# Kernel optimization log

Hardware: AMD Instinct MI355X
Metric: run time of the kernel (lower is better)

## Reference

```python
import jax, jax.numpy as jnp
import numpy as np

B, C, H, W = 32, 64, 64, 64
K, D = 512, 64
COMMITMENT_COST = 0.25


def setup_inputs() -> dict:
    key = jax.random.key(0)
    k1, k2, k3 = jax.random.split(key, 3)
    inputs = jax.random.normal(k1, (B, C, H, W), dtype=jnp.float32)
    codebook0 = jax.random.normal(k2, (K, D), dtype=jnp.float32)
    codebook1 = jax.random.normal(k3, (K, D), dtype=jnp.float32)
    return {"inputs": inputs, "codebook0": codebook0, "codebook1": codebook1, "idx": 1}


def reference(inputs, codebook0, codebook1, idx):
    # NCHW -> NHWC, flatten to [N, D]
    x = jnp.transpose(inputs, (0, 2, 3, 1))
    flat = x.reshape(-1, D)  # [N, D]
    if idx == 0:
        codes = codebook0
    else:
        codes = jnp.concatenate([codebook0, codebook1], axis=0)  # [2K, D]
    # squared-distance matrix [N, 2K]
    distances = (jnp.sum(flat * flat, axis=1, keepdims=True)
                 + jnp.sum(codes * codes, axis=1)
                 - 2.0 * jnp.matmul(flat, codes.T))
    encoding_indices = jnp.argmin(distances, axis=1)  # [N]
    # gather == one-hot @ codes, without materializing one-hot
    quantized = jnp.take(codes, encoding_indices, axis=0).reshape(x.shape)
    sg = jax.lax.stop_gradient
    e_latent_loss = jnp.mean((sg(quantized) - x) ** 2)
    q_latent_loss = jnp.mean((quantized - sg(x)) ** 2)
    loss = q_latent_loss + COMMITMENT_COST * e_latent_loss
    # straight-through estimator
    quantized_st = x + sg(quantized - x)
    # perplexity from usage histogram (== mean of one-hot encodings)
    n = flat.shape[0]
    counts = jnp.zeros((codes.shape[0],), dtype=jnp.float32).at[encoding_indices].add(1.0)
    avg_probs = counts / n
    perplexity = jnp.exp(-jnp.sum(avg_probs * jnp.log(avg_probs + 1e-10)))
    return (jnp.transpose(quantized_st, (0, 3, 1, 2)), loss, perplexity)
```

## Files before the change

### kernel.cpp

```cpp
#include <hip/hip_runtime.h>


typedef __attribute__((ext_vector_type(8))) short short8;
typedef __attribute__((ext_vector_type(16))) float f32x16;

#define LOSS_OFF 0
#define PART_OFF 2048
#define PACKED_OFF 34816
#define NPART 32
#define CHUNK_B 18432

__device__ __forceinline__ unsigned short bf16_rne(float v, float& rest) {
  const unsigned u = __float_as_uint(v);
  const unsigned r = u + 0x7fffu + ((u >> 16) & 1u);
  const unsigned short h = (unsigned short)(r >> 16);
  rest = v - __uint_as_float((unsigned)h << 16);
  return h;
}

__global__ void vq_pack(const float* __restrict__ cb0, const float* __restrict__ cb1,
                        float* __restrict__ ws) {
  const int c = blockIdx.x * 256 + threadIdx.x;
  if (c < NPART) ws[LOSS_OFF + c] = 0.0f;
#pragma unroll
  for (int p = 0; p < NPART; ++p) ws[PART_OFF + p * 1024 + c] = 0.0f;
  const float* row = (c < 512) ? (cb0 + (size_t)c * 64) : (cb1 + (size_t)(c - 512) * 64);
  float v[64];
  float nrm = 0.f;
#pragma unroll
  for (int d = 0; d < 64; d += 4) {
    const float4 f = *(const float4*)(row + d);
    v[d] = f.x; v[d + 1] = f.y; v[d + 2] = f.z; v[d + 3] = f.w;
    nrm += f.x * f.x + f.y * f.y + f.z * f.z + f.w * f.w;
  }
  unsigned short hi[64], lo[64];
#pragma unroll
  for (int d = 0; d < 64; ++d) {
    float rest, dump;
    hi[d] = bf16_rne(v[d], rest);
    lo[d] = bf16_rne(rest, dump);
  }
  float* base = ws + PACKED_OFF + (size_t)(c >> 6) * 4608 + (c & 63) * 4;
#pragma unroll
  for (int g = 0; g < 16; ++g) {
    short8 gr;
#pragma unroll
    for (int e = 0; e < 8; ++e)
      gr[e] = (short)((g < 8) ? hi[g * 8 + e] : lo[(g - 8) * 8 + e]);
    *(short8*)(base + g * 256) = gr;
  }
  {
    const float nh = -0.5f * nrm;
    float r1, r2, dump;
    const unsigned short n0 = bf16_rne(nh, r1);
    const unsigned short n1 = bf16_rne(r1, r2);
    const unsigned short n2 = bf16_rne(r2, dump);
    short8 g16 = {(short)n0, (short)n1, (short)n2, 0, 0, 0, 0, 0};
    *(short8*)(base + 16 * 256) = g16;
    short8 zz = {0, 0, 0, 0, 0, 0, 0, 0};
    *(short8*)(base + 17 * 256) = zz;
  }
}

__global__ __launch_bounds__(256, 2) void vq_dist(
    const float* __restrict__ xin, const int* __restrict__ idxp,
    const float* __restrict__ cb0, const float* __restrict__ cb1,
    float* __restrict__ out, float* __restrict__ ws) {
  __shared__ int qidxL[256];
  const int tid = threadIdx.x;
  const int w = tid >> 6;
  const int l = tid & 63;
  const int half = l >> 5;
  const int col = l & 31;
  const int blk = blockIdx.x;
  const int bb = blk >> 4;
  const int hw0 = (blk & 15) << 8;
  const int nch = (*idxp == 0) ? 8 : 16;

  short8 xh[2][4], xl[2][4];
  float xx[2];
#pragma unroll
  for (int m = 0; m < 2; ++m) {
    float vv[4][8];
    const float* xb =
        xin + ((size_t)(bb * 64 + half * 8)) * 4096 + hw0 + w * 64 + m * 32 + col;
#pragma unroll
    for (int kf = 0; kf < 4; ++kf)
#pragma unroll
      for (int j = 0; j < 8; ++j)
        vv[kf][j] = xb[((size_t)(kf * 16 + j)) * 4096];
    float s = 0.f;
#pragma unroll
    for (int kf = 0; kf < 4; ++kf)
#pragma unroll
      for (int j = 0; j < 8; ++j) {
        const float v = vv[kf][j];
        float rest, dump;
        xh[m][kf][j] = (short)bf16_rne(v, rest);
        xl[m][kf][j] = (short)bf16_rne(rest, dump);
        s += v * v;
      }
    s += __shfl_xor(s, 32);
    xx[m] = s;
  }
  short8 xnh;
#pragma unroll
  for (int j = 0; j < 8; ++j)
    xnh[j] = (short)((half == 0 && j < 3) ? 0x3F80 : 0);
  const f32x16 ZV = (f32x16)0.0f;

  float best[2][16];
#pragma unroll
  for (int m = 0; m < 2; ++m)
#pragma unroll
    for (int r = 0; r < 16; ++r) best[m][r] = -3.4e38f;

  const char* pkl = (const char*)(ws + PACKED_OFF) + col * 16 + half * 1024;

#pragma unroll 2
  for (int i = 0; i < nch; ++i) {
    const char* tb0 = pkl + (size_t)i * CHUNK_B;
    const char* tb1 = tb0 + 512;

    const short8 An0 = *(const short8*)(tb0 + 16 * 1024);
    const short8 An1 = *(const short8*)(tb1 + 16 * 1024);
    f32x16 a00 = __builtin_amdgcn_mfma_f32_32x32x16_bf16(An0, xnh, ZV, 0, 0, 0);
    f32x16 a01 = __builtin_amdgcn_mfma_f32_32x32x16_bf16(An1, xnh, ZV, 0, 0, 0);
    f32x16 a10 = __builtin_amdgcn_mfma_f32_32x32x16_bf16(An0, xnh, ZV, 0, 0, 0);
    f32x16 a11 = __builtin_amdgcn_mfma_f32_32x32x16_bf16(An1, xnh, ZV, 0, 0, 0);
#pragma unroll
    for (int kf = 0; kf < 4; ++kf) {
      const short8 Ah0 = *(const short8*)(tb0 + (2 * kf) * 1024);
      const short8 Ah1 = *(const short8*)(tb1 + (2 * kf) * 1024);
      const short8 Al0 = *(const short8*)(tb0 + (8 + 2 * kf) * 1024);
      const short8 Al1 = *(const short8*)(tb1 + (8 + 2 * kf) * 1024);
      a00 = __builtin_amdgcn_mfma_f32_32x32x16_bf16(Ah0, xh[0][kf], a00, 0, 0, 0);
      a01 = __builtin_amdgcn_mfma_f32_32x32x16_bf16(Ah1, xh[0][kf], a01, 0, 0, 0);
      a10 = __builtin_amdgcn_mfma_f32_32x32x16_bf16(Ah0, xh[1][kf], a10, 0, 0, 0);
      a11 = __builtin_amdgcn_mfma_f32_32x32x16_bf16(Ah1, xh[1][kf], a11, 0, 0, 0);
      a00 = __builtin_amdgcn_mfma_f32_32x32x16_bf16(Ah0, xl[0][kf], a00, 0, 0, 0);
      a01 = __builtin_amdgcn_mfma_f32_32x32x16_bf16(Ah1, xl[0][kf], a01, 0, 0, 0);
      a10 = __builtin_amdgcn_mfma_f32_32x32x16_bf16(Ah0, xl[1][kf], a10, 0, 0, 0);
      a11 = __builtin_amdgcn_mfma_f32_32x32x16_bf16(Ah1, xl[1][kf], a11, 0, 0, 0);
      a00 = __builtin_amdgcn_mfma_f32_32x32x16_bf16(Al0, xh[0][kf], a00, 0, 0, 0);
      a01 = __builtin_amdgcn_mfma_f32_32x32x16_bf16(Al1, xh[0][kf], a01, 0, 0, 0);
      a10 = __builtin_amdgcn_mfma_f32_32x32x16_bf16(Al0, xh[1][kf], a10, 0, 0, 0);
      a11 = __builtin_amdgcn_mfma_f32_32x32x16_bf16(Al1, xh[1][kf], a11, 0, 0, 0);
    }

    const unsigned sid0 = (unsigned)(31 - 2 * i);
    const unsigned sid1 = (unsigned)(30 - 2 * i);
#pragma unroll
    for (int r = 0; r < 16; ++r) {
      const float p00 = __uint_as_float((__float_as_uint(a00[r]) & 0xFFFFFFE0u) | sid0);
      const float p01 = __uint_as_float((__float_as_uint(a01[r]) & 0xFFFFFFE0u) | sid1);
      best[0][r] = fmaxf(fmaxf(p00, p01), best[0][r]);
      const float p10 = __uint_as_float((__float_as_uint(a10[r]) & 0xFFFFFFE0u) | sid0);
      const float p11 = __uint_as_float((__float_as_uint(a11[r]) & 0xFFFFFFE0u) | sid1);
      best[1][r] = fmaxf(fmaxf(p10, p11), best[1][r]);
    }
  }

  float ls = 0.f;
#pragma unroll
  for (int m = 0; m < 2; ++m) {
    float win = best[m][0];
    int wr = 0;
#pragma unroll
    for (int r = 1; r < 16; ++r) {
      const bool g = best[m][r] > win;
      win = g ? best[m][r] : win;
      wr = g ? r : wr;
    }
    const unsigned u = __float_as_uint(win);
    const int t = 31 - (int)(u & 31u);
    int code = (t >> 1) * 64 + (t & 1) * 32 + ((wr & 3) + 8 * (wr >> 2) + 4 * half);
    float clean = __uint_as_float(u & 0xFFFFFFE0u);
    const float ocl = __shfl_xor(clean, 32);
    const int oc = __shfl_xor(code, 32);
    const bool take = (ocl > clean) || (ocl == clean && oc < code);
    clean = take ? ocl : clean;
    code = take ? oc : code;
    if (half == 0) {
      qidxL[w * 64 + m * 32 + col] = code;
      ls += xx[m] - 2.0f * clean;
    }
  }
#pragma unroll
  for (int mk = 1; mk < 64; mk <<= 1) ls += __shfl_xor(ls, mk);
  if (l == 0) atomicAdd(&ws[LOSS_OFF + (blk & (NPART - 1))], ls);
  __syncthreads();

  const int ci = qidxL[tid];
  atomicAdd(ws + PART_OFF + (size_t)(blk & (NPART - 1)) * 1024 + ci, 1.0f);
  const float* crow = (ci < 512) ? (cb0 + (size_t)ci * 64) : (cb1 + (size_t)(ci - 512) * 64);
  float* ob = out + (((size_t)(bb * 64)) << 12) + hw0 + tid;
#pragma unroll
  for (int d4 = 0; d4 < 16; ++d4) {
    const float4 f = *(const float4*)(crow + d4 * 4);
    ob[((size_t)(d4 * 4 + 0)) << 12] = f.x;
    ob[((size_t)(d4 * 4 + 1)) << 12] = f.y;
    ob[((size_t)(d4 * 4 + 2)) << 12] = f.z;
    ob[((size_t)(d4 * 4 + 3)) << 12] = f.w;
  }
}

__global__ void vq_final(const float* __restrict__ ws, float* __restrict__ out) {
  __shared__ float sred[256];
  const int t = threadIdx.x;
  float h = 0.f;
#pragma unroll
  for (int i = t; i < 1024; i += 256) {
    float s = 0.f;
#pragma unroll
    for (int p = 0; p < NPART; ++p) s += ws[PART_OFF + p * 1024 + i];
    const float avg = s * (1.0f / 131072.0f);
    h += avg * logf(avg + 1e-10f);
  }
  sred[t] = h;
  __syncthreads();
  for (int s2 = 128; s2 > 0; s2 >>= 1) {
    if (t < s2) sred[t] += sred[t + s2];
    __syncthreads();
  }
  if (t == 0) {
    float lsum = 0.f;
#pragma unroll
    for (int p = 0; p < NPART; ++p) lsum += ws[LOSS_OFF + p];
    out[8388608] = 1.25f * lsum * (1.0f / 8388608.0f);
    out[8388609] = expf(-sred[0]);
  }
}

extern "C" void kernel_launch(void* const* d_in, const int* in_sizes, int n_in,
                              void* d_out, int out_size, void* d_ws, size_t ws_size,
                              hipStream_t stream) {
  (void)in_sizes; (void)n_in; (void)out_size; (void)ws_size;
  const float* xin = (const float*)d_in[0];
  const float* cb0 = (const float*)d_in[1];
  const float* cb1 = (const float*)d_in[2];
  const int* idxp = (const int*)d_in[3];
  float* out = (float*)d_out;
  float* ws = (float*)d_ws;

  vq_pack<<<4, 256, 0, stream>>>(cb0, cb1, ws);
  vq_dist<<<512, 256, 0, stream>>>(xin, idxp, cb0, cb1, out, ws);
  vq_final<<<1, 256, 0, stream>>>(ws, out);
}
```

Before: 84.24 us.

## Halve per-block tile to 128 points and raise occupancy with more blocks

Each wave now handles one 32-point M tile instead of two, so a block covers 128 spatial positions and the grid doubles to 1024 blocks. Launch bounds go from 2 to 4 blocks per SIMD to cut register pressure and raise occupancy. The output write phase splits the 64 channels across two thread halves. The trade-off is that each loaded codebook fragment is reused by half as many MFMAs, which doubles codebook traffic from L2/L1.

```diff
diff --git a/kernel.cpp b/kernel.cpp
--- a/kernel.cpp
+++ b/kernel.cpp
@@ -62,28 +62,27 @@
   }
 }
 
-__global__ __launch_bounds__(256, 2) void vq_dist(
+__global__ __launch_bounds__(256, 4) void vq_dist(
     const float* __restrict__ xin, const int* __restrict__ idxp,
     const float* __restrict__ cb0, const float* __restrict__ cb1,
     float* __restrict__ out, float* __restrict__ ws) {
-  __shared__ int qidxL[256];
+  __shared__ int qidxL[128];
   const int tid = threadIdx.x;
   const int w = tid >> 6;
   const int l = tid & 63;
   const int half = l >> 5;
   const int col = l & 31;
   const int blk = blockIdx.x;
-  const int bb = blk >> 4;
-  const int hw0 = (blk & 15) << 8;
+  const int bb = blk >> 5;
+  const int hw0 = (blk & 31) << 7;
   const int nch = (*idxp == 0) ? 8 : 16;
 
-  short8 xh[2][4], xl[2][4];
-  float xx[2];
-#pragma unroll
-  for (int m = 0; m < 2; ++m) {
+  short8 xh[4], xl[4];
+  float xx;
+  {
     float vv[4][8];
     const float* xb =
-        xin + ((size_t)(bb * 64 + half * 8)) * 4096 + hw0 + w * 64 + m * 32 + col;
+        xin + ((size_t)(bb * 64 + half * 8)) * 4096 + hw0 + w * 32 + col;
 #pragma unroll
     for (int kf = 0; kf < 4; ++kf)
 #pragma unroll
@@ -96,12 +95,12 @@
       for (int j = 0; j < 8; ++j) {
         const float v = vv[kf][j];
         float rest, dump;
-        xh[m][kf][j] = (short)bf16_rne(v, rest);
-        xl[m][kf][j] = (short)bf16_rne(rest, dump);
+        xh[kf][j] = (short)bf16_rne(v, rest);
+        xl[kf][j] = (short)bf16_rne(rest, dump);
         s += v * v;
       }
     s += __shfl_xor(s, 32);
-    xx[m] = s;
+    xx = s;
   }
   short8 xnh;
 #pragma unroll
@@ -109,11 +108,9 @@
     xnh[j] = (short)((half == 0 && j < 3) ? 0x3F80 : 0);
   const f32x16 ZV = (f32x16)0.0f;
 
-  float best[2][16];
-#pragma unroll
-  for (int m = 0; m < 2; ++m)
-#pragma unroll
-    for (int r = 0; r < 16; ++r) best[m][r] = -3.4e38f;
+  float best[16];
+#pragma unroll
+  for (int r = 0; r < 16; ++r) best[r] = -3.4e38f;
 
   const char* pkl = (const char*)(ws + PACKED_OFF) + col * 16 + half * 1024;
 
@@ -124,52 +121,40 @@
 
     const short8 An0 = *(const short8*)(tb0 + 16 * 1024);
     const short8 An1 = *(const short8*)(tb1 + 16 * 1024);
-    f32x16 a00 = __builtin_amdgcn_mfma_f32_32x32x16_bf16(An0, xnh, ZV, 0, 0, 0);
-    f32x16 a01 = __builtin_amdgcn_mfma_f32_32x32x16_bf16(An1, xnh, ZV, 0, 0, 0);
-    f32x16 a10 = __builtin_amdgcn_mfma_f32_32x32x16_bf16(An0, xnh, ZV, 0, 0, 0);
-    f32x16 a11 = __builtin_amdgcn_mfma_f32_32x32x16_bf16(An1, xnh, ZV, 0, 0, 0);
+    f32x16 a0 = __builtin_amdgcn_mfma_f32_32x32x16_bf16(An0, xnh, ZV, 0, 0, 0);
+    f32x16 a1 = __builtin_amdgcn_mfma_f32_32x32x16_bf16(An1, xnh, ZV, 0, 0, 0);
 #pragma unroll
     for (int kf = 0; kf < 4; ++kf) {
       const short8 Ah0 = *(const short8*)(tb0 + (2 * kf) * 1024);
       const short8 Ah1 = *(const short8*)(tb1 + (2 * kf) * 1024);
       const short8 Al0 = *(const short8*)(tb0 + (8 + 2 * kf) * 1024);
       const short8 Al1 = *(const short8*)(tb1 + (8 + 2 * kf) * 1024);
-      a00 = __builtin_amdgcn_mfma_f32_32x32x16_bf16(Ah0, xh[0][kf], a00, 0, 0, 0);
-      a01 = __builtin_amdgcn_mfma_f32_32x32x16_bf16(Ah1, xh[0][kf], a01, 0, 0, 0);
-      a10 = __builtin_amdgcn_mfma_f32_32x32x16_bf16(Ah0, xh[1][kf], a10, 0, 0, 0);
-      a11 = __builtin_amdgcn_mfma_f32_32x32x16_bf16(Ah1, xh[1][kf], a11, 0, 0, 0);
-      a00 = __builtin_amdgcn_mfma_f32_32x32x16_bf16(Ah0, xl[0][kf], a00, 0, 0, 0);
-      a01 = __builtin_amdgcn_mfma_f32_32x32x16_bf16(Ah1, xl[0][kf], a01, 0, 0, 0);
-      a10 = __builtin_amdgcn_mfma_f32_32x32x16_bf16(Ah0, xl[1][kf], a10, 0, 0, 0);
-      a11 = __builtin_amdgcn_mfma_f32_32x32x16_bf16(Ah1, xl[1][kf], a11, 0, 0, 0);
-      a00 = __builtin_amdgcn_mfma_f32_32x32x16_bf16(Al0, xh[0][kf], a00, 0, 0, 0);
-      a01 = __builtin_amdgcn_mfma_f32_32x32x16_bf16(Al1, xh[0][kf], a01, 0, 0, 0);
-      a10 = __builtin_amdgcn_mfma_f32_32x32x16_bf16(Al0, xh[1][kf], a10, 0, 0, 0);
-      a11 = __builtin_amdgcn_mfma_f32_32x32x16_bf16(Al1, xh[1][kf], a11, 0, 0, 0);
+      a0 = __builtin_amdgcn_mfma_f32_32x32x16_bf16(Ah0, xh[kf], a0, 0, 0, 0);
+      a1 = __builtin_amdgcn_mfma_f32_32x32x16_bf16(Ah1, xh[kf], a1, 0, 0, 0);
+      a0 = __builtin_amdgcn_mfma_f32_32x32x16_bf16(Ah0, xl[kf], a0, 0, 0, 0);
+      a1 = __builtin_amdgcn_mfma_f32_32x32x16_bf16(Ah1, xl[kf], a1, 0, 0, 0);
+      a0 = __builtin_amdgcn_mfma_f32_32x32x16_bf16(Al0, xh[kf], a0, 0, 0, 0);
+      a1 = __builtin_amdgcn_mfma_f32_32x32x16_bf16(Al1, xh[kf], a1, 0, 0, 0);
     }
 
     const unsigned sid0 = (unsigned)(31 - 2 * i);
     const unsigned sid1 = (unsigned)(30 - 2 * i);
 #pragma unroll
     for (int r = 0; r < 16; ++r) {
-      const float p00 = __uint_as_float((__float_as_uint(a00[r]) & 0xFFFFFFE0u) | sid0);
-      const float p01 = __uint_as_float((__float_as_uint(a01[r]) & 0xFFFFFFE0u) | sid1);
-      best[0][r] = fmaxf(fmaxf(p00, p01), best[0][r]);
-      const float p10 = __uint_as_float((__float_as_uint(a10[r]) & 0xFFFFFFE0u) | sid0);
-      const float p11 = __uint_as_float((__float_as_uint(a11[r]) & 0xFFFFFFE0u) | sid1);
-      best[1][r] = fmaxf(fmaxf(p10, p11), best[1][r]);
+      const float p0 = __uint_as_float((__float_as_uint(a0[r]) & 0xFFFFFFE0u) | sid0);
+      const float p1 = __uint_as_float((__float_as_uint(a1[r]) & 0xFFFFFFE0u) | sid1);
+      best[r] = fmaxf(fmaxf(p0, p1), best[r]);
     }
   }
 
   float ls = 0.f;
-#pragma unroll
-  for (int m = 0; m < 2; ++m) {
-    float win = best[m][0];
+  {
+    float win = best[0];
     int wr = 0;
 #pragma unroll
     for (int r = 1; r < 16; ++r) {
-      const bool g = best[m][r] > win;
-      win = g ? best[m][r] : win;
+      const bool g = best[r] > win;
+      win = g ? best[r] : win;
       wr = g ? r : wr;
     }
     const unsigned u = __float_as_uint(win);
@@ -182,8 +167,8 @@
     clean = take ? ocl : clean;
     code = take ? oc : code;
     if (half == 0) {
-      qidxL[w * 64 + m * 32 + col] = code;
-      ls += xx[m] - 2.0f * clean;
+      qidxL[w * 32 + col] = code;
+      ls = xx - 2.0f * clean;
     }
   }
 #pragma unroll
@@ -191,18 +176,20 @@
   if (l == 0) atomicAdd(&ws[LOSS_OFF + (blk & (NPART - 1))], ls);
   __syncthreads();
 
-  const int ci = qidxL[tid];
-  atomicAdd(ws + PART_OFF + (size_t)(blk & (NPART - 1)) * 1024 + ci, 1.0f);
+  const int q = tid & 127;
+  const int dh = tid >> 7;
+  const int ci = qidxL[q];
+  if (tid < 128) atomicAdd(ws + PART_OFF + (size_t)(blk & (NPART - 1)) * 1024 + ci, 1.0f);
   const float* crow = (ci < 512) ? (cb0 + (size_t)ci * 64) : (cb1 + (size_t)(ci - 512) * 64);
-  float* ob = out + (((size_t)(bb * 64)) << 12) + hw0 + tid;
-#pragma unroll
-  for (int d4 = 0; d4 < 16; ++d4) {
-    const float4 f = *(const float4*)(crow + d4 * 4);
-    ob[((size_t)(d4 * 4 + 0)) << 12] = f.x;
-    ob[((size_t)(d4 * 4 + 1)) << 12] = f.y;
-    ob[((size_t)(d4 * 4 + 2)) << 12] = f.z;
-    ob[((size_t)(d4 * 4 + 3)) << 12] = f.w;
-  }
+  float cv[32];
+#pragma unroll
+  for (int d = 0; d < 32; d += 4) {
+    const float4 f = *(const float4*)(crow + dh * 32 + d);
+    cv[d] = f.x; cv[d + 1] = f.y; cv[d + 2] = f.z; cv[d + 3] = f.w;
+  }
+  float* ob = out + (((size_t)(bb * 64 + dh * 32)) << 12) + hw0 + q;
+#pragma unroll
+  for (int d = 0; d < 32; ++d) ob[(size_t)d << 12] = cv[d];
 }
 
 __global__ void vq_final(const float* __restrict__ ws, float* __restrict__ out) {
@@ -244,6 +231,6 @@
   float* ws = (float*)d_ws;
 
   vq_pack<<<4, 256, 0, stream>>>(cb0, cb1, ws);
-  vq_dist<<<512, 256, 0, stream>>>(xin, idxp, cb0, cb1, out, ws);
+  vq_dist<<<1024, 256, 0, stream>>>(xin, idxp, cb0, cb1, out, ws);
   vq_final<<<1, 256, 0, stream>>>(ws, out);
 }
```

New measurement: 92.74 us. +10.1%, slower.
